# Performance work log

Measured on AMD Instinct MI355X. Metric: run time of the kernel, lower is better.

## Reference

```python
import jax, jax.numpy as jnp
import numpy as np

EPS = 1e-8


def setup_inputs() -> dict:
    key = jax.random.key(0)
    k1, k2, k3, k4, k5 = jax.random.split(key, 5)
    B, N_LOG, N_PHYS, E = 16, 512, 2048, 2048
    P = jax.random.uniform(k1, (B, N_LOG, N_PHYS), dtype=jnp.float32)
    d_hw = jax.random.randint(k2, (N_PHYS, N_PHYS), 0, 4, dtype=jnp.int32)
    edge_src = jax.random.randint(k3, (B, E), 0, N_LOG, dtype=jnp.int32)
    edge_dst = jax.random.randint(k4, (B, E), 0, N_LOG, dtype=jnp.int32)
    edge_w = jax.random.uniform(k5, (B, E), dtype=jnp.float32)
    return {"P": P, "d_hw": d_hw, "edge_src": edge_src,
            "edge_dst": edge_dst, "edge_w": edge_w}


def reference(P, d_hw, edge_src, edge_dst, edge_w):
    # A_hw[p,q] = 1 where hardware distance == 1 (adjacent qubits)
    A_hw = (d_hw == 1).astype(P.dtype)                      # [Q, Q]
    B = P.shape[0]
    # Dense contraction once per batch: PA[b,i,q] = sum_p P[b,i,p] A[p,q]
    PA = jnp.einsum('bip,pq->biq', P, A_hw)                 # [B, N, Q]
    b_idx = jnp.arange(B)[:, None]                          # [B, 1]
    gi = PA[b_idx, edge_src]                                # [B, E, Q]
    gj = P[b_idx, edge_dst]                                 # [B, E, Q]
    adj_score = jnp.einsum('beq,beq->be', gi, gj)           # [B, E]
    sample_adj = jnp.sum(edge_w * adj_score, axis=-1)       # [B]
    sample_weight = jnp.maximum(jnp.sum(edge_w, axis=-1), EPS)
    # every sample has edges -> valid_samples = B
    loss = -jnp.mean(sample_adj / sample_weight)
    return loss
```

## Files before the change

### kernel.cpp

```cpp
#include <hip/hip_runtime.h>
#include <hip/hip_bf16.h>

#define BATCH 16
#define NLOG 512
#define Q 2048
#define NEDGE 2048
#define M_TOT (BATCH * NLOG)
#define KB 2048
#define EDOT_BLOCKS 256

typedef float f32x2 __attribute__((ext_vector_type(2)));
typedef float f32x4 __attribute__((ext_vector_type(4)));
typedef int i32x4 __attribute__((ext_vector_type(4)));
typedef int i32x8 __attribute__((ext_vector_type(8)));

__device__ __forceinline__ unsigned char to_e4m3(float f) {
    int pk = __builtin_amdgcn_cvt_pk_fp8_f32(f, f, 0, false);
    return (unsigned char)(pk & 0xff);
}

__device__ __forceinline__ float dot16(i32x4 a, i32x4 b) {
    float s0 = 0.f, s1 = 0.f;
    #pragma unroll
    for (int d = 0; d < 4; d++) {
        f32x2 alo = __builtin_amdgcn_cvt_pk_f32_fp8(a[d], false);
        f32x2 ahi = __builtin_amdgcn_cvt_pk_f32_fp8(a[d], true);
        f32x2 blo = __builtin_amdgcn_cvt_pk_f32_fp8(b[d], false);
        f32x2 bhi = __builtin_amdgcn_cvt_pk_f32_fp8(b[d], true);
        s0 += alo[0] * blo[0] + alo[1] * blo[1];
        s1 += ahi[0] * bhi[0] + ahi[1] * bhi[1];
    }
    return s0 + s1;
}

__global__ __launch_bounds__(256) void prep(const float* __restrict__ P,
                                            unsigned char* __restrict__ P8,
                                            const int* __restrict__ d_hw,
                                            unsigned char* __restrict__ A8t,
                                            float* __restrict__ adj,
                                            float* __restrict__ wsum,
                                            unsigned* __restrict__ counter) {
    int bid = blockIdx.x;
    if (bid == 0) {
        if (threadIdx.x == 0) *counter = 0u;
        if (threadIdx.x < BATCH) { adj[threadIdx.x] = 0.f; wsum[threadIdx.x] = 0.f; }
    }
    if (bid < 8192) {
        int i = (bid * 256 + threadIdx.x) * 8;
        float4 v0 = *(const float4*)(P + i);
        float4 v1 = *(const float4*)(P + i + 4);
        int lo = 0, hi = 0;
        lo = __builtin_amdgcn_cvt_pk_fp8_f32(v0.x, v0.y, lo, false);
        lo = __builtin_amdgcn_cvt_pk_fp8_f32(v0.z, v0.w, lo, true);
        hi = __builtin_amdgcn_cvt_pk_fp8_f32(v1.x, v1.y, hi, false);
        hi = __builtin_amdgcn_cvt_pk_fp8_f32(v1.z, v1.w, hi, true);
        int2 st; st.x = lo; st.y = hi;
        *(int2*)(P8 + i) = st;
    } else {
        bid -= 8192;
        __shared__ unsigned char tile[32][33];
        int q0 = (bid & 63) * 32;
        int p0 = (bid >> 6) * 32;
        int tx = threadIdx.x & 31;
        int ty = threadIdx.x >> 5;
        for (int s = 0; s < 32; s += 8) {
            int p = p0 + ty + s;
            int v = d_hw[(size_t)p * Q + q0 + tx];
            tile[ty + s][tx] = (v == 1) ? 0x38 : 0x00;
        }
        __syncthreads();
        for (int s = 0; s < 32; s += 8) {
            A8t[(size_t)(q0 + ty + s) * Q + p0 + tx] = tile[tx][ty + s];
        }
    }
}

#define GSTAGE(bufAs, bufBs, kk0)                                              \
    {                                                                          \
        _Pragma("unroll")                                                      \
        for (int c = 0; c < 4; c++) {                                          \
            const unsigned char* g =                                           \
                A + (size_t)(m0 + c * 64 + s_row) * KB + (kk0) + s_off;        \
            __builtin_amdgcn_global_load_lds(                                  \
                (const __attribute__((address_space(1))) void*)g,              \
                (__attribute__((address_space(3))) void*)((bufAs) + c * 8192 + t * 16), \
                16, 0, 0);                                                     \
        }                                                                      \
        _Pragma("unroll")                                                      \
        for (int c = 0; c < 4; c++) {                                          \
            const unsigned char* g =                                           \
                Bt + (size_t)(n0 + c * 64 + s_row) * KB + (kk0) + s_off;       \
            __builtin_amdgcn_global_load_lds(                                  \
                (const __attribute__((address_space(1))) void*)g,              \
                (__attribute__((address_space(3))) void*)((bufBs) + c * 8192 + t * 16), \
                16, 0, 0);                                                     \
        }                                                                      \
    }

#define GCOMPUTE(bufAs, bufBs)                                                 \
    {                                                                          \
        i32x8 bfr[4];                                                          \
        _Pragma("unroll")                                                      \
        for (int j = 0; j < 4; j++) {                                          \
            int base = (wc * 64 + j * 16 + lane16) << 7;                       \
            i32x4 lo = *(const i32x4*)((bufBs) + base + c0);                   \
            i32x4 hi = *(const i32x4*)((bufBs) + base + c1);                   \
            bfr[j] = __builtin_shufflevector(lo, hi, 0, 1, 2, 3, 4, 5, 6, 7);  \
        }                                                                      \
        _Pragma("unroll")                                                      \
        for (int i = 0; i < 8; i++) {                                          \
            int base = (wr * 128 + i * 16 + lane16) << 7;                      \
            i32x4 lo = *(const i32x4*)((bufAs) + base + c0);                   \
            i32x4 hi = *(const i32x4*)((bufAs) + base + c1);                   \
            i32x8 af = __builtin_shufflevector(lo, hi, 0, 1, 2, 3, 4, 5, 6, 7);\
            _Pragma("unroll")                                                  \
            for (int j = 0; j < 4; j++)                                        \
                acc[i][j] = __builtin_amdgcn_mfma_scale_f32_16x16x128_f8f6f4(  \
                    af, bfr[j], acc[i][j], 0, 0, 0, 127, 0, 127);              \
        }                                                                      \
    }

__global__ __launch_bounds__(512, 2) void gemm_bt8(const unsigned char* __restrict__ A,
                                                   const unsigned char* __restrict__ Bt,
                                                   unsigned char* __restrict__ PA8) {
    __shared__ unsigned char As[2][32768];
    __shared__ unsigned char Bs[2][32768];

    const int t = threadIdx.x;
    const int w = t >> 6;
    const int wr = w >> 2, wc = w & 3;
    const int l = t & 63;
    const int quad = l >> 4;
    const int lane16 = l & 15;

    const int m0 = blockIdx.x * 256;
    const int n0 = blockIdx.y * 256;

    const int s_row = t >> 3;
    const int s_off = (((t & 7) ^ (s_row & 7)) << 4);

    const int r7 = lane16 & 7;
    const int c0 = ((2 * quad) ^ r7) << 4;
    const int c1 = ((2 * quad + 1) ^ r7) << 4;

    f32x4 acc[8][4] = {};

    GSTAGE(As[0], Bs[0], 0);
    __syncthreads();

    for (int kk = 0; kk < 15; kk++) {
        const int cur = kk & 1;
        GSTAGE(As[cur ^ 1], Bs[cur ^ 1], (kk + 1) * 128);
        GCOMPUTE(As[cur], Bs[cur]);
        __syncthreads();
    }
    GCOMPUTE(As[1], Bs[1]);

    #pragma unroll
    for (int i = 0; i < 8; i++) {
        #pragma unroll
        for (int j = 0; j < 4; j++) {
            #pragma unroll
            for (int r = 0; r < 4; r++) {
                int row = m0 + wr * 128 + i * 16 + quad * 4 + r;
                int col = n0 + wc * 64 + j * 16 + lane16;
                PA8[(size_t)row * Q + col] = to_e4m3(acc[i][j][r] * (1.0f / 256.0f));
            }
        }
    }
}

__global__ __launch_bounds__(512) void edge_dot(const unsigned char* __restrict__ PA8,
                                                const unsigned char* __restrict__ P8,
                                                const int* __restrict__ esrc,
                                                const int* __restrict__ edst,
                                                const float* __restrict__ ew,
                                                float* __restrict__ adj,
                                                float* __restrict__ wsum,
                                                unsigned* __restrict__ counter,
                                                float* __restrict__ out) {
    const int lid = blockIdx.x;
    const int b = (lid & 7) | ((lid >> 7) << 3);
    const int chunk = (lid >> 3) & 15;
    const int t = threadIdx.x;
    const int w = t >> 6;
    const int lane = t & 63;

    const int e0 = b * NEDGE + chunk * 128 + w * 16;
    const unsigned char* Ab = PA8 + (size_t)b * NLOG * Q;
    const unsigned char* Bb = P8  + (size_t)b * NLOG * Q;
    const int off = lane * 32;

    int src = esrc[e0], dst = edst[e0];
    float wcur = ew[e0];
    const unsigned char* ap = Ab + (size_t)src * Q + off;
    const unsigned char* bp = Bb + (size_t)dst * Q + off;
    i32x4 A0 = *(const i32x4*)ap;
    i32x4 A1 = *(const i32x4*)(ap + 16);
    i32x4 B0 = *(const i32x4*)bp;
    i32x4 B1 = *(const i32x4*)(bp + 16);

    float acc = 0.f;
    float wacc = 0.f;
    #pragma unroll
    for (int e = 0; e < 16; e++) {
        i32x4 nA0 = A0, nA1 = A1, nB0 = B0, nB1 = B1;
        float wnext = 0.f;
        if (e < 15) {
            int ns = esrc[e0 + e + 1], nd = edst[e0 + e + 1];
            wnext = ew[e0 + e + 1];
            const unsigned char* nap = Ab + (size_t)ns * Q + off;
            const unsigned char* nbp = Bb + (size_t)nd * Q + off;
            nA0 = *(const i32x4*)nap;
            nA1 = *(const i32x4*)(nap + 16);
            nB0 = *(const i32x4*)nbp;
            nB1 = *(const i32x4*)(nbp + 16);
        }
        float p = dot16(A0, B0) + dot16(A1, B1);
        acc += wcur * p;
        wacc += wcur;
        A0 = nA0; A1 = nA1; B0 = nB0; B1 = nB1; wcur = wnext;
    }

    #pragma unroll
    for (int o = 32; o > 0; o >>= 1) acc += __shfl_xor(acc, o);

    __shared__ float ra[8], rw[8];
    if (lane == 0) { ra[w] = acc; rw[w] = wacc; }
    __syncthreads();

    if (t == 0) {
        float a = 0.f, ws = 0.f;
        #pragma unroll
        for (int i = 0; i < 8; i++) { a += ra[i]; ws += rw[i]; }
        atomicAdd(&adj[b],  a * 256.0f);
        atomicAdd(&wsum[b], ws);
        __threadfence();
        if (atomicAdd(counter, 1u) == EDOT_BLOCKS - 1) {
            __threadfence();
            float s = 0.f;
            #pragma unroll
            for (int bb = 0; bb < BATCH; bb++) {
                float av = atomicAdd(&adj[bb], 0.0f);
                float wv = atomicAdd(&wsum[bb], 0.0f);
                s += av / fmaxf(wv, 1e-8f);
            }
            out[0] = -s / (float)BATCH;
        }
    }
}

extern "C" void kernel_launch(void* const* d_in, const int* in_sizes, int n_in,
                              void* d_out, int out_size, void* d_ws, size_t ws_size,
                              hipStream_t stream) {
    const float* P    = (const float*)d_in[0];
    const int* d_hw   = (const int*)d_in[1];
    const int* esrc   = (const int*)d_in[2];
    const int* edst   = (const int*)d_in[3];
    const float* ew   = (const float*)d_in[4];
    float* out        = (float*)d_out;

    char* ws = (char*)d_ws;
    unsigned char* P8  = (unsigned char*)ws;
    unsigned char* A8t = (unsigned char*)(ws + 16777216);
    unsigned char* PA8 = (unsigned char*)(ws + 20971520);
    float* adj         = (float*)(ws + 37748736);
    float* wsum        = (float*)(ws + 37748736 + 64);
    unsigned* counter  = (unsigned*)(ws + 37748736 + 128);

    prep<<<8192 + 4096, 256, 0, stream>>>(P, P8, d_hw, A8t, adj, wsum, counter);
    gemm_bt8<<<dim3(M_TOT / 256, Q / 256), 512, 0, stream>>>(P8, A8t, PA8);
    edge_dot<<<EDOT_BLOCKS, 512, 0, stream>>>(PA8, P8, esrc, edst, ew, adj, wsum, counter, out);
}
```

Measured before the change: 172.8 us.

## Interleave global-to-LDS staging with MFMA clusters using barriers and setprio

Restructures the fp8 GEMM main loop so the next tile's global_load_lds copies are split into small groups and issued between four clusters of MFMAs. Each cluster is bracketed by s_barrier and s_setprio to keep waves in lockstep and favour the matrix instructions. An explicit vmcnt(0) wait replaces __syncthreads before the buffer swap. The aim is to hide load latency and LDS-read stalls behind matrix math. The cost is more barriers per iteration and reliance on hand-written waitcnt for correctness.

After: 170.3 us. Within noise of the previous version (-1.5%).

```diff
diff --git a/kernel.cpp b/kernel.cpp
--- a/kernel.cpp
+++ b/kernel.cpp
@@ -75,50 +75,27 @@
     }
 }
 
-#define GSTAGE(bufAs, bufBs, kk0)                                              \
-    {                                                                          \
-        _Pragma("unroll")                                                      \
-        for (int c = 0; c < 4; c++) {                                          \
-            const unsigned char* g =                                           \
-                A + (size_t)(m0 + c * 64 + s_row) * KB + (kk0) + s_off;        \
-            __builtin_amdgcn_global_load_lds(                                  \
-                (const __attribute__((address_space(1))) void*)g,              \
-                (__attribute__((address_space(3))) void*)((bufAs) + c * 8192 + t * 16), \
-                16, 0, 0);                                                     \
-        }                                                                      \
-        _Pragma("unroll")                                                      \
-        for (int c = 0; c < 4; c++) {                                          \
-            const unsigned char* g =                                           \
-                Bt + (size_t)(n0 + c * 64 + s_row) * KB + (kk0) + s_off;       \
-            __builtin_amdgcn_global_load_lds(                                  \
-                (const __attribute__((address_space(1))) void*)g,              \
-                (__attribute__((address_space(3))) void*)((bufBs) + c * 8192 + t * 16), \
-                16, 0, 0);                                                     \
-        }                                                                      \
-    }
-
-#define GCOMPUTE(bufAs, bufBs)                                                 \
-    {                                                                          \
-        i32x8 bfr[4];                                                          \
-        _Pragma("unroll")                                                      \
-        for (int j = 0; j < 4; j++) {                                          \
-            int base = (wc * 64 + j * 16 + lane16) << 7;                       \
-            i32x4 lo = *(const i32x4*)((bufBs) + base + c0);                   \
-            i32x4 hi = *(const i32x4*)((bufBs) + base + c1);                   \
-            bfr[j] = __builtin_shufflevector(lo, hi, 0, 1, 2, 3, 4, 5, 6, 7);  \
-        }                                                                      \
-        _Pragma("unroll")                                                      \
-        for (int i = 0; i < 8; i++) {                                          \
-            int base = (wr * 128 + i * 16 + lane16) << 7;                      \
-            i32x4 lo = *(const i32x4*)((bufAs) + base + c0);                   \
-            i32x4 hi = *(const i32x4*)((bufAs) + base + c1);                   \
-            i32x8 af = __builtin_shufflevector(lo, hi, 0, 1, 2, 3, 4, 5, 6, 7);\
-            _Pragma("unroll")                                                  \
-            for (int j = 0; j < 4; j++)                                        \
-                acc[i][j] = __builtin_amdgcn_mfma_scale_f32_16x16x128_f8f6f4(  \
-                    af, bfr[j], acc[i][j], 0, 0, 0, 127, 0, 127);              \
-        }                                                                      \
-    }
+#define MF(af, bf, accv) __builtin_amdgcn_mfma_scale_f32_16x16x128_f8f6f4( \
+    (af), (bf), (accv), 0, 0, 0, 127, 0, 127)
+
+#define READ_FRAG(buf, rowbase) __extension__({                                \
+    const int _b = ((rowbase) + lane16) << 7;                                  \
+    i32x4 _lo = *(const i32x4*)((buf) + _b + c0);                              \
+    i32x4 _hi = *(const i32x4*)((buf) + _b + c1);                              \
+    __builtin_shufflevector(_lo, _hi, 0, 1, 2, 3, 4, 5, 6, 7); })
+
+#define SA(dstbuf, c, kk0)                                                     \
+    __builtin_amdgcn_global_load_lds(                                          \
+        (const __attribute__((address_space(1))) void*)(A +                    \
+            (size_t)(m0 + (c) * 64 + s_row) * KB + (kk0) + s_off),             \
+        (__attribute__((address_space(3))) void*)((dstbuf) + (c) * 8192 + t * 16), \
+        16, 0, 0)
+#define SBst(dstbuf, c, kk0)                                                   \
+    __builtin_amdgcn_global_load_lds(                                          \
+        (const __attribute__((address_space(1))) void*)(Bt +                   \
+            (size_t)(n0 + (c) * 64 + s_row) * KB + (kk0) + s_off),             \
+        (__attribute__((address_space(3))) void*)((dstbuf) + (c) * 8192 + t * 16), \
+        16, 0, 0)
 
 __global__ __launch_bounds__(512, 2) void gemm_bt8(const unsigned char* __restrict__ A,
                                                    const unsigned char* __restrict__ Bt,
@@ -145,16 +122,72 @@
 
     f32x4 acc[8][4] = {};
 
-    GSTAGE(As[0], Bs[0], 0);
+    {
+        SA(As[0], 0, 0); SA(As[0], 1, 0); SA(As[0], 2, 0); SA(As[0], 3, 0);
+        SBst(Bs[0], 0, 0); SBst(Bs[0], 1, 0); SBst(Bs[0], 2, 0); SBst(Bs[0], 3, 0);
+    }
     __syncthreads();
 
-    for (int kk = 0; kk < 15; kk++) {
-        const int cur = kk & 1;
-        GSTAGE(As[cur ^ 1], Bs[cur ^ 1], (kk + 1) * 128);
-        GCOMPUTE(As[cur], Bs[cur]);
-        __syncthreads();
-    }
-    GCOMPUTE(As[1], Bs[1]);
+    for (int kt = 0; kt < 16; ++kt) {
+        const unsigned char* as = As[kt & 1];
+        const unsigned char* bs = Bs[kt & 1];
+        unsigned char* an = As[(kt + 1) & 1];
+        unsigned char* bn = Bs[(kt + 1) & 1];
+        const int kn = (kt + 1) * 128;
+        const bool st = (kt < 15);
+
+        i32x8 bf0 = READ_FRAG(bs, wc * 64 + 0);
+        i32x8 bf1 = READ_FRAG(bs, wc * 64 + 16);
+        i32x8 bf2 = READ_FRAG(bs, wc * 64 + 32);
+        i32x8 bf3 = READ_FRAG(bs, wc * 64 + 48);
+        i32x8 af0 = READ_FRAG(as, wr * 128 + 0);
+        i32x8 af1 = READ_FRAG(as, wr * 128 + 16);
+        if (st) { SA(an, 0, kn); SA(an, 1, kn); SA(an, 2, kn); }
+        __builtin_amdgcn_s_barrier();
+        __builtin_amdgcn_s_setprio(1);
+        acc[0][0] = MF(af0, bf0, acc[0][0]); acc[0][1] = MF(af0, bf1, acc[0][1]);
+        acc[0][2] = MF(af0, bf2, acc[0][2]); acc[0][3] = MF(af0, bf3, acc[0][3]);
+        acc[1][0] = MF(af1, bf0, acc[1][0]); acc[1][1] = MF(af1, bf1, acc[1][1]);
+        acc[1][2] = MF(af1, bf2, acc[1][2]); acc[1][3] = MF(af1, bf3, acc[1][3]);
+        __builtin_amdgcn_s_setprio(0);
+        __builtin_amdgcn_s_barrier();
+
+        i32x8 af2 = READ_FRAG(as, wr * 128 + 32);
+        i32x8 af3 = READ_FRAG(as, wr * 128 + 48);
+        if (st) { SA(an, 3, kn); SBst(bn, 0, kn); SBst(bn, 1, kn); }
+        __builtin_amdgcn_s_barrier();
+        __builtin_amdgcn_s_setprio(1);
+        acc[2][0] = MF(af2, bf0, acc[2][0]); acc[2][1] = MF(af2, bf1, acc[2][1]);
+        acc[2][2] = MF(af2, bf2, acc[2][2]); acc[2][3] = MF(af2, bf3, acc[2][3]);
+        acc[3][0] = MF(af3, bf0, acc[3][0]); acc[3][1] = MF(af3, bf1, acc[3][1]);
+        acc[3][2] = MF(af3, bf2, acc[3][2]); acc[3][3] = MF(af3, bf3, acc[3][3]);
+        __builtin_amdgcn_s_setprio(0);
+        __builtin_amdgcn_s_barrier();
+
+        i32x8 af4 = READ_FRAG(as, wr * 128 + 64);
+        i32x8 af5 = READ_FRAG(as, wr * 128 + 80);
+        if (st) { SBst(bn, 2, kn); SBst(bn, 3, kn); }
+        __builtin_amdgcn_s_barrier();
+        __builtin_amdgcn_s_setprio(1);
+        acc[4][0] = MF(af4, bf0, acc[4][0]); acc[4][1] = MF(af4, bf1, acc[4][1]);
+        acc[4][2] = MF(af4, bf2, acc[4][2]); acc[4][3] = MF(af4, bf3, acc[4][3]);
+        acc[5][0] = MF(af5, bf0, acc[5][0]); acc[5][1] = MF(af5, bf1, acc[5][1]);
+        acc[5][2] = MF(af5, bf2, acc[5][2]); acc[5][3] = MF(af5, bf3, acc[5][3]);
+        __builtin_amdgcn_s_setprio(0);
+        __builtin_amdgcn_s_barrier();
+
+        i32x8 af6 = READ_FRAG(as, wr * 128 + 96);
+        i32x8 af7 = READ_FRAG(as, wr * 128 + 112);
+        __builtin_amdgcn_s_barrier();
+        __builtin_amdgcn_s_setprio(1);
+        acc[6][0] = MF(af6, bf0, acc[6][0]); acc[6][1] = MF(af6, bf1, acc[6][1]);
+        acc[6][2] = MF(af6, bf2, acc[6][2]); acc[6][3] = MF(af6, bf3, acc[6][3]);
+        acc[7][0] = MF(af7, bf0, acc[7][0]); acc[7][1] = MF(af7, bf1, acc[7][1]);
+        acc[7][2] = MF(af7, bf2, acc[7][2]); acc[7][3] = MF(af7, bf3, acc[7][3]);
+        __builtin_amdgcn_s_setprio(0);
+        asm volatile("s_waitcnt vmcnt(0)" ::: "memory");
+        __builtin_amdgcn_s_barrier();
+    }
 
     #pragma unroll
     for (int i = 0; i < 8; i++) {
```
